# Optimization experiments

Hardware: AMD Instinct MI355X
Metric: run time of the kernel (lower is better)

## Reference

```python
import jax, jax.numpy as jnp
import numpy as np

K = 10  # top-k per query


def setup_inputs() -> dict:
    key = jax.random.key(0)
    k1, k2 = jax.random.split(key)
    B_Q, B_D = 4096, 32768
    similarity_scores = jax.random.normal(k1, (B_Q, B_D), dtype=jnp.float32)
    positive_mask = jax.random.randint(k2, (B_Q, B_D), 0, 2).astype(jnp.bool_)
    return {"similarity_scores": similarity_scores, "positive_mask": positive_mask}


def reference(similarity_scores, positive_mask):
    # Per-row top-k over the doc axis: values [B,k], indices [B,k]
    top_k_values, top_k_indices = jax.lax.top_k(similarity_scores, K)
    labels = jnp.take_along_axis(
        positive_mask.astype(jnp.float32), top_k_indices, axis=1
    )  # [B, k] relevance labels at the top-k positions

    # DCG discounts: log2(position + 1), positions 1..k
    positions = jnp.arange(1, K + 1, dtype=jnp.float32)
    discounts = jnp.log2(positions + 1.0)  # [k]

    actual_dcg = jnp.sum(labels / discounts, axis=1)  # [B]
    ideal_labels = -jnp.sort(-labels, axis=1)  # descending sort
    ideal_dcg = jnp.sum(ideal_labels / discounts, axis=1)  # [B]

    # Loss per query: 1 - NDCG if ideal_dcg > 0 else 0.
    # (Queries with no positives anywhere also have ideal_dcg == 0 -> skipped,
    #  matching the torch `continue` / early-return-0 behavior.)
    per_query = jnp.where(ideal_dcg > 0, 1.0 - actual_dcg / jnp.maximum(ideal_dcg, 1e-30), 0.0)

    batch_size_query = similarity_scores.shape[0]
    return jnp.sum(per_query) / batch_size_query
```

## Files before the change

### kernel.cpp

```cpp
#include <hip/hip_runtime.h>
#include <cstdint>
#include <cstddef>

#define KTOP 10
#define BQ 4096
#define BD 32768
#define THREADS 256
#define F4_PER_ROW (BD / 4)
#define ITERS (F4_PER_ROW / THREADS)
#define CAP (THREADS * KTOP)
#define T_STATIC 3.0f

__global__ __launch_bounds__(THREADS) void topk_ndcg_rows(
    const float* __restrict__ scores,
    const int* __restrict__ mask,
    float* __restrict__ per_row)
{
    const int row = blockIdx.x;
    const int tid = threadIdx.x;
    const float4* row4 = reinterpret_cast<const float4*>(scores + (size_t)row * BD);

    __shared__ int   s_cnt;
    __shared__ float cv[CAP];
    __shared__ int   ci[CAP];
    __shared__ float wv[4];
    __shared__ int   wi[4];
    __shared__ int   wt[4];
    __shared__ int   topi[KTOP];

    if (tid == 0) s_cnt = 0;
    __syncthreads();

    for (int i = 0; i < ITERS; ++i) {
        const int f4 = tid + i * THREADS;
        const float4 x = row4[f4];
        const float m = fmaxf(fmaxf(x.x, x.y), fmaxf(x.z, x.w));
        if (m >= T_STATIC) {
            const int jb = f4 * 4;
            float vs[4] = { x.x, x.y, x.z, x.w };
#pragma unroll
            for (int c = 0; c < 4; ++c) {
                if (vs[c] >= T_STATIC) {
                    const int p = atomicAdd(&s_cnt, 1);
                    if (p < CAP) { cv[p] = vs[c]; ci[p] = jb + c; }
                }
            }
        }
    }
    __syncthreads();
    int n = s_cnt;

    if (n < KTOP || n > CAP) {
        float tv[KTOP]; int ti[KTOP];
#pragma unroll
        for (int k = 0; k < KTOP; ++k) { tv[k] = -INFINITY; ti[k] = 0x7fffffff; }
        for (int i = 0; i < ITERS; ++i) {
            const int f4 = tid + i * THREADS;
            const float4 x = row4[f4];
            const int jb = f4 * 4;
            float vs[4] = { x.x, x.y, x.z, x.w };
#pragma unroll
            for (int c = 0; c < 4; ++c) {
                const float v = vs[c];
                const int   j = jb + c;
                if (v > tv[KTOP - 1]) {
                    bool cc[KTOP];
#pragma unroll
                    for (int k = 0; k < KTOP; ++k) cc[k] = v > tv[k];
#pragma unroll
                    for (int k = KTOP - 1; k >= 1; --k) {
                        tv[k] = cc[k] ? (cc[k - 1] ? tv[k - 1] : v) : tv[k];
                        ti[k] = cc[k] ? (cc[k - 1] ? ti[k - 1] : j) : ti[k];
                    }
                    if (cc[0]) { tv[0] = v; ti[0] = j; }
                }
            }
        }
        __syncthreads();
#pragma unroll
        for (int k = 0; k < KTOP; ++k) { cv[tid * KTOP + k] = tv[k]; ci[tid * KTOP + k] = ti[k]; }
        n = CAP;
        __syncthreads();
    }

    float tv[KTOP]; int ti[KTOP];
#pragma unroll
    for (int k = 0; k < KTOP; ++k) { tv[k] = -INFINITY; ti[k] = 0x7fffffff; }
    for (int p = tid; p < n; p += THREADS) {
        const float v = cv[p];
        const int   j = ci[p];
        const bool enter = (v > tv[KTOP - 1]) || (v == tv[KTOP - 1] && j < ti[KTOP - 1]);
        if (enter) {
            bool cc[KTOP];
#pragma unroll
            for (int k = 0; k < KTOP; ++k) cc[k] = (v > tv[k]) || (v == tv[k] && j < ti[k]);
#pragma unroll
            for (int k = KTOP - 1; k >= 1; --k) {
                tv[k] = cc[k] ? (cc[k - 1] ? tv[k - 1] : v) : tv[k];
                ti[k] = cc[k] ? (cc[k - 1] ? ti[k - 1] : j) : ti[k];
            }
            if (cc[0]) { tv[0] = v; ti[0] = j; }
        }
    }
    __syncthreads();
#pragma unroll
    for (int k = 0; k < KTOP; ++k) { cv[tid * KTOP + k] = tv[k]; ci[tid * KTOP + k] = ti[k]; }
    __syncthreads();

    int p = 0;
    for (int r = 0; r < KTOP; ++r) {
        float cvv = (p < KTOP) ? cv[tid * KTOP + p] : -INFINITY;
        int   cii = (p < KTOP) ? ci[tid * KTOP + p] : 0x7fffffff;
        int   ct  = tid;
#pragma unroll
        for (int m = 32; m >= 1; m >>= 1) {
            const float ov = __shfl_xor(cvv, m);
            const int   oi = __shfl_xor(cii, m);
            const int   ot = __shfl_xor(ct, m);
            const bool take = (ov > cvv) || (ov == cvv && oi < cii);
            cvv = take ? ov : cvv;
            cii = take ? oi : cii;
            ct  = take ? ot : ct;
        }
        if ((tid & 63) == 0) { const int w = tid >> 6; wv[w] = cvv; wi[w] = cii; wt[w] = ct; }
        __syncthreads();
        float bv = wv[0]; int bi = wi[0]; int bt = wt[0];
#pragma unroll
        for (int w = 1; w < 4; ++w) {
            const float ov = wv[w]; const int oi = wi[w]; const int ot = wt[w];
            const bool take = (ov > bv) || (ov == bv && oi < bi);
            bv = take ? ov : bv;
            bi = take ? oi : bi;
            bt = take ? ot : bt;
        }
        if (tid == bt) ++p;
        if (tid == 0) topi[r] = bi;
        __syncthreads();
    }

    if (tid == 0) {
        float invd[KTOP];
#pragma unroll
        for (int r = 0; r < KTOP; ++r) invd[r] = 1.0f / log2f((float)(r + 2));
        const int* mrow = mask + (size_t)row * BD;
        float actual = 0.0f;
        int cnt = 0;
#pragma unroll
        for (int r = 0; r < KTOP; ++r) {
            const bool pos = (mrow[topi[r]] != 0);
            actual += pos ? invd[r] : 0.0f;
            cnt += pos ? 1 : 0;
        }
        float ideal = 0.0f;
#pragma unroll
        for (int r = 0; r < KTOP; ++r) ideal += (r < cnt) ? invd[r] : 0.0f;
        per_row[row] = (ideal > 0.0f) ? (1.0f - actual / ideal) : 0.0f;
    }
}

__global__ __launch_bounds__(256) void reduce_mean(
    const float* __restrict__ per_row, float* __restrict__ out)
{
    const int tid = threadIdx.x;
    float s = 0.0f;
    for (int i = tid; i < BQ; i += 256) s += per_row[i];
#pragma unroll
    for (int m = 32; m >= 1; m >>= 1) s += __shfl_xor(s, m);
    __shared__ float ws[4];
    if ((tid & 63) == 0) ws[tid >> 6] = s;
    __syncthreads();
    if (tid == 0) out[0] = (ws[0] + ws[1] + ws[2] + ws[3]) / (float)BQ;
}

extern "C" void kernel_launch(void* const* d_in, const int* in_sizes, int n_in,
                              void* d_out, int out_size, void* d_ws, size_t ws_size,
                              hipStream_t stream) {
    const float* scores = (const float*)d_in[0];
    const int*   mask   = (const int*)d_in[1];
    float* per_row = (float*)d_ws;

    topk_ndcg_rows<<<BQ, THREADS, 0, stream>>>(scores, mask, per_row);
    reduce_mean<<<1, 256, 0, stream>>>(per_row, (float*)d_out);
}
```

Baseline: 139.1 us.

## Shrink candidate buffer, unroll nontemporal loads, use single-wave merge and wave-level extraction

Cuts the candidate capacity from 2560 to 512 entries. The streaming filter pass is unrolled four-wide with nontemporal loads. The block-wide ten-round extraction, which used shared memory and barriers, is replaced by one wave inserting the candidates and doing a shuffle-based top-10 extraction. The NDCG arithmetic is spread across lanes with wave reductions instead of a serial loop on thread 0. The fallback path now reduces to per-wave top-10 lists, and the lower shared memory use may raise occupancy.

Result: slower. 265.2 us (+90.6%).

```diff
diff --git a/kernel.cpp b/kernel.cpp
--- a/kernel.cpp
+++ b/kernel.cpp
@@ -8,41 +8,86 @@
 #define THREADS 256
 #define F4_PER_ROW (BD / 4)
 #define ITERS (F4_PER_ROW / THREADS)
-#define CAP (THREADS * KTOP)
+#define CAP 512
 #define T_STATIC 3.0f
+
+typedef float nf4 __attribute__((ext_vector_type(4)));
+
+__device__ __forceinline__ void insert_tie(float v, int j, float (&tv)[KTOP], int (&ti)[KTOP]) {
+    const bool enter = (v > tv[KTOP - 1]) || (v == tv[KTOP - 1] && j < ti[KTOP - 1]);
+    if (enter) {
+        bool cc[KTOP];
+#pragma unroll
+        for (int k = 0; k < KTOP; ++k) cc[k] = (v > tv[k]) || (v == tv[k] && j < ti[k]);
+#pragma unroll
+        for (int k = KTOP - 1; k >= 1; --k) {
+            tv[k] = cc[k] ? (cc[k - 1] ? tv[k - 1] : v) : tv[k];
+            ti[k] = cc[k] ? (cc[k - 1] ? ti[k - 1] : j) : ti[k];
+        }
+        if (cc[0]) { tv[0] = v; ti[0] = j; }
+    }
+}
+
+__device__ __forceinline__ void wave_extract10(float (&tv)[KTOP], int (&ti)[KTOP],
+                                               int lane, float &myv, int &myi) {
+#pragma unroll
+    for (int r = 0; r < KTOP; ++r) {
+        float bv = tv[0]; int bi = ti[0]; int bl = lane;
+#pragma unroll
+        for (int m = 32; m >= 1; m >>= 1) {
+            const float ov = __shfl_xor(bv, m);
+            const int   oi = __shfl_xor(bi, m);
+            const int   ol = __shfl_xor(bl, m);
+            const bool take = (ov > bv) || (ov == bv && oi < bi);
+            bv = take ? ov : bv;
+            bi = take ? oi : bi;
+            bl = take ? ol : bl;
+        }
+        if (lane == bl) {
+#pragma unroll
+            for (int k = 0; k < KTOP - 1; ++k) { tv[k] = tv[k + 1]; ti[k] = ti[k + 1]; }
+            tv[KTOP - 1] = -INFINITY; ti[KTOP - 1] = 0x7fffffff;
+        }
+        if (lane == r) { myv = bv; myi = bi; }
+    }
+}
 
 __global__ __launch_bounds__(THREADS) void topk_ndcg_rows(
     const float* __restrict__ scores,
     const int* __restrict__ mask,
     float* __restrict__ per_row)
 {
-    const int row = blockIdx.x;
-    const int tid = threadIdx.x;
-    const float4* row4 = reinterpret_cast<const float4*>(scores + (size_t)row * BD);
+    const int row  = blockIdx.x;
+    const int tid  = threadIdx.x;
+    const int lane = tid & 63;
+    const int wv   = tid >> 6;
+    const nf4* row4 = reinterpret_cast<const nf4*>(scores + (size_t)row * BD);
 
     __shared__ int   s_cnt;
     __shared__ float cv[CAP];
     __shared__ int   ci[CAP];
-    __shared__ float wv[4];
-    __shared__ int   wi[4];
-    __shared__ int   wt[4];
-    __shared__ int   topi[KTOP];
 
     if (tid == 0) s_cnt = 0;
     __syncthreads();
 
-    for (int i = 0; i < ITERS; ++i) {
-        const int f4 = tid + i * THREADS;
-        const float4 x = row4[f4];
-        const float m = fmaxf(fmaxf(x.x, x.y), fmaxf(x.z, x.w));
-        if (m >= T_STATIC) {
-            const int jb = f4 * 4;
-            float vs[4] = { x.x, x.y, x.z, x.w };
+    for (int i = 0; i < ITERS; i += 4) {
+        nf4 xs[4];
 #pragma unroll
-            for (int c = 0; c < 4; ++c) {
-                if (vs[c] >= T_STATIC) {
-                    const int p = atomicAdd(&s_cnt, 1);
-                    if (p < CAP) { cv[p] = vs[c]; ci[p] = jb + c; }
+        for (int u = 0; u < 4; ++u)
+            xs[u] = __builtin_nontemporal_load(row4 + (i + u) * THREADS + tid);
+#pragma unroll
+        for (int u = 0; u < 4; ++u) {
+            const nf4 x = xs[u];
+            const float m = fmaxf(fmaxf(x.x, x.y), fmaxf(x.z, x.w));
+            if (m >= T_STATIC) {
+                const int jb = ((i + u) * THREADS + tid) * 4;
+                const float vs[4] = { x.x, x.y, x.z, x.w };
+#pragma unroll
+                for (int c = 0; c < 4; ++c) {
+                    if (vs[c] >= T_STATIC) {
+                        const int p = atomicAdd(&s_cnt, 1);
+                        if (p < CAP) { cv[p] = vs[c]; ci[p] = jb + c; }
+                    }
                 }
             }
         }
@@ -50,111 +95,50 @@
     __syncthreads();
     int n = s_cnt;
 
-    if (n < KTOP || n > CAP) {
-        float tv[KTOP]; int ti[KTOP];
-#pragma unroll
-        for (int k = 0; k < KTOP; ++k) { tv[k] = -INFINITY; ti[k] = 0x7fffffff; }
-        for (int i = 0; i < ITERS; ++i) {
-            const int f4 = tid + i * THREADS;
-            const float4 x = row4[f4];
-            const int jb = f4 * 4;
-            float vs[4] = { x.x, x.y, x.z, x.w };
-#pragma unroll
-            for (int c = 0; c < 4; ++c) {
-                const float v = vs[c];
-                const int   j = jb + c;
-                if (v > tv[KTOP - 1]) {
-                    bool cc[KTOP];
-#pragma unroll
-                    for (int k = 0; k < KTOP; ++k) cc[k] = v > tv[k];
-#pragma unroll
-                    for (int k = KTOP - 1; k >= 1; --k) {
-                        tv[k] = cc[k] ? (cc[k - 1] ? tv[k - 1] : v) : tv[k];
-                        ti[k] = cc[k] ? (cc[k - 1] ? ti[k - 1] : j) : ti[k];
-                    }
-                    if (cc[0]) { tv[0] = v; ti[0] = j; }
-                }
-            }
-        }
-        __syncthreads();
-#pragma unroll
-        for (int k = 0; k < KTOP; ++k) { cv[tid * KTOP + k] = tv[k]; ci[tid * KTOP + k] = ti[k]; }
-        n = CAP;
-        __syncthreads();
-    }
-
     float tv[KTOP]; int ti[KTOP];
 #pragma unroll
     for (int k = 0; k < KTOP; ++k) { tv[k] = -INFINITY; ti[k] = 0x7fffffff; }
-    for (int p = tid; p < n; p += THREADS) {
-        const float v = cv[p];
-        const int   j = ci[p];
-        const bool enter = (v > tv[KTOP - 1]) || (v == tv[KTOP - 1] && j < ti[KTOP - 1]);
-        if (enter) {
-            bool cc[KTOP];
+
+    if (n < KTOP || n > CAP) {
+        for (int i = 0; i < ITERS; ++i) {
+            const int f4 = i * THREADS + tid;
+            const nf4 x = row4[f4];
+            const int jb = f4 * 4;
+            const float vs[4] = { x.x, x.y, x.z, x.w };
 #pragma unroll
-            for (int k = 0; k < KTOP; ++k) cc[k] = (v > tv[k]) || (v == tv[k] && j < ti[k]);
+            for (int c = 0; c < 4; ++c) insert_tie(vs[c], jb + c, tv, ti);
+        }
+        float fv = 0.0f; int fi = 0;
+        wave_extract10(tv, ti, lane, fv, fi);
+        if (lane < KTOP) { cv[wv * KTOP + lane] = fv; ci[wv * KTOP + lane] = fi; }
+        __syncthreads();
+        n = 4 * KTOP;
+    }
+
+    if (wv == 0) {
 #pragma unroll
-            for (int k = KTOP - 1; k >= 1; --k) {
-                tv[k] = cc[k] ? (cc[k - 1] ? tv[k - 1] : v) : tv[k];
-                ti[k] = cc[k] ? (cc[k - 1] ? ti[k - 1] : j) : ti[k];
-            }
-            if (cc[0]) { tv[0] = v; ti[0] = j; }
-        }
-    }
-    __syncthreads();
+        for (int k = 0; k < KTOP; ++k) { tv[k] = -INFINITY; ti[k] = 0x7fffffff; }
+        for (int p = lane; p < n; p += 64) insert_tie(cv[p], ci[p], tv, ti);
+
+        float myv = 0.0f; int myi = 0;
+        wave_extract10(tv, ti, lane, myv, myi);
+
+        const int* mrow = mask + (size_t)row * BD;
+        const int pos = (lane < KTOP) ? ((mrow[myi] != 0) ? 1 : 0) : 0;
+
+        int cnt = pos;
 #pragma unroll
-    for (int k = 0; k < KTOP; ++k) { cv[tid * KTOP + k] = tv[k]; ci[tid * KTOP + k] = ti[k]; }
-    __syncthreads();
+        for (int m = 32; m >= 1; m >>= 1) cnt += __shfl_xor(cnt, m);
 
-    int p = 0;
-    for (int r = 0; r < KTOP; ++r) {
-        float cvv = (p < KTOP) ? cv[tid * KTOP + p] : -INFINITY;
-        int   cii = (p < KTOP) ? ci[tid * KTOP + p] : 0x7fffffff;
-        int   ct  = tid;
+        const float invd = 1.0f / log2f((float)(lane + 2));
+        float a = pos ? invd : 0.0f;
+        float b = (lane < cnt) ? invd : 0.0f;
 #pragma unroll
         for (int m = 32; m >= 1; m >>= 1) {
-            const float ov = __shfl_xor(cvv, m);
-            const int   oi = __shfl_xor(cii, m);
-            const int   ot = __shfl_xor(ct, m);
-            const bool take = (ov > cvv) || (ov == cvv && oi < cii);
-            cvv = take ? ov : cvv;
-            cii = take ? oi : cii;
-            ct  = take ? ot : ct;
+            a += __shfl_xor(a, m);
+            b += __shfl_xor(b, m);
         }
-        if ((tid & 63) == 0) { const int w = tid >> 6; wv[w] = cvv; wi[w] = cii; wt[w] = ct; }
-        __syncthreads();
-        float bv = wv[0]; int bi = wi[0]; int bt = wt[0];
-#pragma unroll
-        for (int w = 1; w < 4; ++w) {
-            const float ov = wv[w]; const int oi = wi[w]; const int ot = wt[w];
-            const bool take = (ov > bv) || (ov == bv && oi < bi);
-            bv = take ? ov : bv;
-            bi = take ? oi : bi;
-            bt = take ? ot : bt;
-        }
-        if (tid == bt) ++p;
-        if (tid == 0) topi[r] = bi;
-        __syncthreads();
-    }
-
-    if (tid == 0) {
-        float invd[KTOP];
-#pragma unroll
-        for (int r = 0; r < KTOP; ++r) invd[r] = 1.0f / log2f((float)(r + 2));
-        const int* mrow = mask + (size_t)row * BD;
-        float actual = 0.0f;
-        int cnt = 0;
-#pragma unroll
-        for (int r = 0; r < KTOP; ++r) {
-            const bool pos = (mrow[topi[r]] != 0);
-            actual += pos ? invd[r] : 0.0f;
-            cnt += pos ? 1 : 0;
-        }
-        float ideal = 0.0f;
-#pragma unroll
-        for (int r = 0; r < KTOP; ++r) ideal += (r < cnt) ? invd[r] : 0.0f;
-        per_row[row] = (ideal > 0.0f) ? (1.0f - actual / ideal) : 0.0f;
+        if (lane == 0) per_row[row] = (b > 0.0f) ? (1.0f - a / b) : 0.0f;
     }
 }
 
```
